# Kernel tuning notes

Measured on AMD Instinct MI355X. Metric: run time of the kernel, lower is better.

## Reference

```python
import jax, jax.numpy as jnp
import numpy as np

D = 1024


def setup_inputs() -> dict:
    key = jax.random.key(0)
    kx, kq, kk, kv, ko = jax.random.split(key, 5)
    scale = 0.02
    x = jax.random.normal(kx, (4, 2048, D), dtype=jnp.float32)
    Wq = jax.random.normal(kq, (D, D), dtype=jnp.float32) * scale
    Wk = jax.random.normal(kk, (D, D), dtype=jnp.float32) * scale
    Wv = jax.random.normal(kv, (D, D), dtype=jnp.float32) * scale
    Wo = jax.random.normal(ko, (D, D), dtype=jnp.float32) * scale
    return {"x": x, "Wq": Wq, "Wk": Wk, "Wv": Wv, "Wo": Wo}


def reference(x, Wq, Wk, Wv, Wo):
    # Linear projections (torch Linear: y = x @ W.T, no bias)
    q = jnp.einsum('bsd,ed->bse', x, Wq)
    k = jnp.einsum('bsd,ed->bse', x, Wk)
    v = jnp.einsum('bsd,ed->bse', x, Wv)
    d = x.shape[-1]
    # HRR binding: circular convolution of k and v along feature dim (rfft domain)
    Fk = jnp.fft.rfft(k, axis=-1)
    Fv = jnp.fft.rfft(v, axis=-1)
    Fq = jnp.fft.rfft(q, axis=-1)
    Fkv = Fk * Fv                      # bound key-value pairs, Fourier domain
    # causal cumulative memory over sequence; FFT is linear so cumsum commutes
    Fmem = jnp.cumsum(Fkv, axis=-2)    # [b, s, d//2+1] complex
    # unbind with query: circular correlation = multiply by conj(rfft(q))
    values_hat = jnp.fft.irfft(Fmem * jnp.conj(Fq), n=d, axis=-1)
    return jnp.einsum('bsd,ed->bse', values_hat, Wo)
```

## Files before the change

kernel.cpp:

```cpp
#include <hip/hip_runtime.h>

#define D_DIM 1024
#define NF 513
#define NB 4
#define NS 2048
#define NTOK (NB * NS)
#define NCH 32
#define CHS (NS / NCH)

typedef __attribute__((ext_vector_type(8))) short short8_t;
typedef __attribute__((ext_vector_type(4))) float f32x4;

__device__ inline unsigned short f2bf(float f) {
    unsigned u = __builtin_bit_cast(unsigned, f);
    u += 0x7FFFu + ((u >> 16) & 1u);
    return (unsigned short)(u >> 16);
}
__device__ inline float bf2f(unsigned short h) {
    unsigned u = ((unsigned)h) << 16;
    return __builtin_bit_cast(float, u);
}
__device__ inline unsigned pkc(float re, float im) {
    return (unsigned)f2bf(re) | ((unsigned)f2bf(im) << 16);
}
__device__ inline float2 upc(unsigned u) {
    return make_float2(bf2f((unsigned short)(u & 0xFFFFu)), bf2f((unsigned short)(u >> 16)));
}

__global__ __launch_bounds__(256) void convert_x(const float* __restrict__ src,
                                                 unsigned short* __restrict__ dst,
                                                 int n4) {
    int i = blockIdx.x * 256 + threadIdx.x;
    int stride = gridDim.x * 256;
    for (; i < n4; i += stride) {
        float4 v = reinterpret_cast<const float4*>(src)[i];
        ushort4 o;
        o.x = f2bf(v.x); o.y = f2bf(v.y); o.z = f2bf(v.z); o.w = f2bf(v.w);
        reinterpret_cast<ushort4*>(dst)[i] = o;
    }
}

__global__ __launch_bounds__(256) void convert_w(const float* __restrict__ Wq,
                                                 const float* __restrict__ Wk,
                                                 const float* __restrict__ Wv,
                                                 const float* __restrict__ Wo,
                                                 unsigned short* __restrict__ Wqkv,
                                                 unsigned short* __restrict__ Wob) {
    int y = blockIdx.y;
    const float* src = (y == 0) ? Wq : (y == 1) ? Wk : (y == 2) ? Wv : Wo;
    unsigned short* dst = (y < 3) ? (Wqkv + (size_t)y * 1048576) : Wob;
    int i = blockIdx.x * 256 + threadIdx.x;
    float4 v = reinterpret_cast<const float4*>(src)[i];
    ushort4 o;
    o.x = f2bf(v.x); o.y = f2bf(v.y); o.z = f2bf(v.z); o.w = f2bf(v.w);
    reinterpret_cast<ushort4*>(dst)[i] = o;
}

#define BM 128
#define BN 128
#define BK 32

__device__ inline void gload_lds16(const void* g, void* l) {
    __builtin_amdgcn_global_load_lds(
        (const __attribute__((address_space(1))) void*)g,
        (__attribute__((address_space(3))) void*)l,
        16, 0, 0);
}

template <typename OutT>
__global__ __launch_bounds__(256) void gemm_bf16_nt(const unsigned short* __restrict__ A,
                                                    const unsigned short* __restrict__ B,
                                                    OutT* __restrict__ C,
                                                    int M, int N, int K) {
    __shared__ __attribute__((aligned(16))) unsigned short ldsA[3 * BM * BK];
    __shared__ __attribute__((aligned(16))) unsigned short ldsB[3 * BM * BK];
    const int tid  = threadIdx.x;
    const int wave = tid >> 6;
    const int lane = tid & 63;
    const int l15  = lane & 15;
    const int k8   = (((lane >> 4) ^ ((l15 >> 1) & 3)) << 3);
    const int wm   = (wave >> 1) * 64;
    const int wn   = (wave & 1) * 64;
    const int bm   = blockIdx.x * BM;
    const int bn   = blockIdx.y * BN;
    const int crow = tid >> 2;
    const int ccol = (((tid & 3) ^ ((tid >> 3) & 3)) << 3);
    const int NT   = K / BK;

    const unsigned short* Arow = A + (size_t)(bm + crow) * K + ccol;
    const unsigned short* Brow = B + (size_t)(bn + crow) * K + ccol;
    const size_t rstep = (size_t)64 * K;

    f32x4 acc[4][4];
#pragma unroll
    for (int i = 0; i < 4; ++i)
#pragma unroll
        for (int j = 0; j < 4; ++j)
            acc[i][j] = (f32x4){0.f, 0.f, 0.f, 0.f};

    auto STAGE = [&](int t, int b) {
        const int k0 = t * BK;
        unsigned short* la = &ldsA[b * (BM * BK) + (tid >> 2) * BK + ((tid & 3) << 3)];
        unsigned short* lb = &ldsB[b * (BM * BK) + (tid >> 2) * BK + ((tid & 3) << 3)];
        gload_lds16(Arow + k0, la);
        gload_lds16(Brow + k0, lb);
        gload_lds16(Arow + rstep + k0, la + 64 * BK);
        gload_lds16(Brow + rstep + k0, lb + 64 * BK);
    };

    STAGE(0, 0);
    STAGE(1, 1);

    for (int j = 0; j < NT; ++j) {
        const int buf = j % 3;
        if (j + 2 < NT) STAGE(j + 2, (j + 2) % 3);

        if (j + 2 < NT)      asm volatile("s_waitcnt vmcnt(8)" ::: "memory");
        else if (j + 1 < NT) asm volatile("s_waitcnt vmcnt(4)" ::: "memory");
        else                 asm volatile("s_waitcnt vmcnt(0)" ::: "memory");
        __builtin_amdgcn_s_barrier();
        asm volatile("" ::: "memory");

        const unsigned short* la = &ldsA[buf * (BM * BK)];
        const unsigned short* lb = &ldsB[buf * (BM * BK)];
        short8_t af[4], bfv[4];
#pragma unroll
        for (int mi = 0; mi < 4; ++mi)
            af[mi] = *reinterpret_cast<const short8_t*>(&la[(wm + mi * 16 + l15) * BK + k8]);
#pragma unroll
        for (int ni = 0; ni < 4; ++ni)
            bfv[ni] = *reinterpret_cast<const short8_t*>(&lb[(wn + ni * 16 + l15) * BK + k8]);

        __builtin_amdgcn_s_setprio(1);
#pragma unroll
        for (int mi = 0; mi < 4; ++mi)
#pragma unroll
            for (int ni = 0; ni < 4; ++ni)
                acc[mi][ni] = __builtin_amdgcn_mfma_f32_16x16x32_bf16(af[mi], bfv[ni], acc[mi][ni], 0, 0, 0);
        __builtin_amdgcn_s_setprio(0);

        __builtin_amdgcn_s_barrier();
        asm volatile("" ::: "memory");
    }

#pragma unroll
    for (int mi = 0; mi < 4; ++mi) {
        int rbase = bm + wm + mi * 16 + (lane >> 4) * 4;
#pragma unroll
        for (int ni = 0; ni < 4; ++ni) {
            int col = bn + wn + ni * 16 + l15;
#pragma unroll
            for (int j = 0; j < 4; ++j) {
                float v = acc[mi][ni][j];
                if constexpr (sizeof(OutT) == 4)
                    C[(size_t)(rbase + j) * N + col] = v;
                else
                    C[(size_t)(rbase + j) * N + col] = f2bf(v);
            }
        }
    }
}

__device__ inline int sw(int i) { return i ^ ((i >> 4) & 15); }

__device__ inline int dr4(int n) {
    return ((n & 3) << 8) | (((n >> 2) & 3) << 6) | (((n >> 4) & 3) << 4) |
           (((n >> 6) & 3) << 2) | ((n >> 8) & 3);
}

__device__ inline float2 cmul(float2 a, float2 b) {
    return make_float2(a.x * b.x - a.y * b.y, a.x * b.y + a.y * b.x);
}

__device__ inline void fft1024_r4(float2* X, const float2* tw, int t) {
#pragma unroll
    for (int s = 0; s < 5; ++s) {
        const int L = 1 << (2 * s);
        const int r = t & (L - 1);
        const int base = ((t >> (2 * s)) << (2 * s + 2)) + r;
        float2 A  = X[sw(base)];
        float2 Bv = X[sw(base + L)];
        float2 Cv = X[sw(base + 2 * L)];
        float2 Dv = X[sw(base + 3 * L)];
        if (s != 0) {
            const int step = 1024 >> (2 * s + 2);
            Bv = cmul(Bv, tw[sw(r * step)]);
            Cv = cmul(Cv, tw[sw(2 * r * step)]);
            Dv = cmul(Dv, tw[sw(3 * r * step)]);
        }
        float2 e0 = make_float2(A.x + Cv.x, A.y + Cv.y);
        float2 e1 = make_float2(A.x - Cv.x, A.y - Cv.y);
        float2 o0 = make_float2(Bv.x + Dv.x, Bv.y + Dv.y);
        float2 o1 = make_float2(Bv.x - Dv.x, Bv.y - Dv.y);
        X[sw(base)]         = make_float2(e0.x + o0.x, e0.y + o0.y);
        X[sw(base + L)]     = make_float2(e1.x + o1.y, e1.y - o1.x);
        X[sw(base + 2 * L)] = make_float2(e0.x - o0.x, e0.y - o0.y);
        X[sw(base + 3 * L)] = make_float2(e1.x - o1.y, e1.y + o1.x);
        __syncthreads();
    }
}

__global__ __launch_bounds__(256) void twiddle_init(float2* __restrict__ twg) {
    int k = blockIdx.x * 256 + threadIdx.x;
    if (k < 768) {
        float ang = -6.283185307179586f * (float)k / 1024.0f;
        float s, c;
        sincosf(ang, &s, &c);
        twg[sw(k)] = make_float2(c, s);
    }
}

__global__ __launch_bounds__(256) void hrr_fft_fwd(const unsigned short* __restrict__ QKV,
                                                   const float2* __restrict__ twg,
                                                   unsigned* __restrict__ Fkv,
                                                   unsigned* __restrict__ Fq) {
    __shared__ __attribute__((aligned(16))) float2 X[1024];
    __shared__ __attribute__((aligned(16))) float2 twL[768];
    const int tid = threadIdx.x;
    const int t0 = blockIdx.x * 2, t1 = t0 + 1;
    for (int i = tid; i < 384; i += 256)
        reinterpret_cast<float4*>(twL)[i] = reinterpret_cast<const float4*>(twg)[i];

#pragma unroll
    for (int which = 0; which < 2; ++which) {
        const int tok = which ? t1 : t0;
        const ushort4* Kr = (const ushort4*)(QKV + (size_t)tok * 3072 + 1024);
        const ushort4* Vr = (const ushort4*)(QKV + (size_t)tok * 3072 + 2048);
        ushort4 k4 = Kr[tid], v4 = Vr[tid];
        X[sw(dr4(4 * tid + 0))] = make_float2(bf2f(k4.x), bf2f(v4.x));
        X[sw(dr4(4 * tid + 1))] = make_float2(bf2f(k4.y), bf2f(v4.y));
        X[sw(dr4(4 * tid + 2))] = make_float2(bf2f(k4.z), bf2f(v4.z));
        X[sw(dr4(4 * tid + 3))] = make_float2(bf2f(k4.w), bf2f(v4.w));
        __syncthreads();
        fft1024_r4(X, twL, tid);
        for (int j = tid; j < NF; j += 256) {
            float2 Zj = X[sw(j)];
            float2 Zm = X[sw((1024 - j) & 1023)];
            float2 Fk = make_float2(0.5f * (Zj.x + Zm.x), 0.5f * (Zj.y - Zm.y));
            float2 Fv = make_float2(0.5f * (Zj.y + Zm.y), 0.5f * (Zm.x - Zj.x));
            float2 p = cmul(Fk, Fv);
            Fkv[(size_t)tok * NF + j] = pkc(p.x, p.y);
        }
        __syncthreads();
    }
    {
        const ushort4* Q0 = (const ushort4*)(QKV + (size_t)t0 * 3072);
        const ushort4* Q1 = (const ushort4*)(QKV + (size_t)t1 * 3072);
        ushort4 a4 = Q0[tid], b4 = Q1[tid];
        X[sw(dr4(4 * tid + 0))] = make_float2(bf2f(a4.x), bf2f(b4.x));
        X[sw(dr4(4 * tid + 1))] = make_float2(bf2f(a4.y), bf2f(b4.y));
        X[sw(dr4(4 * tid + 2))] = make_float2(bf2f(a4.z), bf2f(b4.z));
        X[sw(dr4(4 * tid + 3))] = make_float2(bf2f(a4.w), bf2f(b4.w));
        __syncthreads();
        fft1024_r4(X, twL, tid);
        for (int j = tid; j < NF; j += 256) {
            float2 Zj = X[sw(j)];
            float2 Zm = X[sw((1024 - j) & 1023)];
            Fq[(size_t)t0 * NF + j] = pkc(0.5f * (Zj.x + Zm.x), 0.5f * (Zj.y - Zm.y));
            Fq[(size_t)t1 * NF + j] = pkc(0.5f * (Zj.y + Zm.y), 0.5f * (Zm.x - Zj.x));
        }
    }
}

__global__ __launch_bounds__(256) void hrr_chunk_sum(const unsigned* __restrict__ Fkv,
                                                     float2* __restrict__ part) {
    int f = blockIdx.x * 256 + threadIdx.x;
    if (f >= NF) return;
    int ch = blockIdx.y, b = blockIdx.z;
    float sx = 0.f, sy = 0.f;
    size_t base = ((size_t)b * NS + (size_t)ch * CHS) * NF + f;
    for (int i = 0; i < CHS; ++i) {
        float2 t = upc(Fkv[base + (size_t)i * NF]);
        sx += t.x; sy += t.y;
    }
    part[(size_t)(b * NCH + ch) * NF + f] = make_float2(sx, sy);
}

__global__ __launch_bounds__(256) void hrr_scan_apply(unsigned* __restrict__ Fkv,
                                                      const unsigned* __restrict__ Fq,
                                                      const float2* __restrict__ part) {
    int f = blockIdx.x * 256 + threadIdx.x;
    if (f >= NF) return;
    int ch = blockIdx.y, b = blockIdx.z;
    float rx = 0.f, ry = 0.f;
    for (int c2 = 0; c2 < ch; ++c2) {
        float2 p = part[(size_t)(b * NCH + c2) * NF + f];
        rx += p.x; ry += p.y;
    }
    size_t base = ((size_t)b * NS + (size_t)ch * CHS) * NF + f;
    for (int i = 0; i < CHS; ++i) {
        size_t idx = base + (size_t)i * NF;
        float2 kv = upc(Fkv[idx]);
        rx += kv.x; ry += kv.y;
        float2 q = upc(Fq[idx]);
        Fkv[idx] = pkc(rx * q.x + ry * q.y, ry * q.x - rx * q.y);
    }
}

__global__ __launch_bounds__(256) void hrr_ifft(const unsigned* __restrict__ U,
                                                const float2* __restrict__ twg,
                                                unsigned short* __restrict__ vhat) {
    __shared__ __attribute__((aligned(16))) float2 X[1024];
    __shared__ __attribute__((aligned(16))) float2 twL[768];
    const int tid = threadIdx.x;
    const int t0 = blockIdx.x * 2, t1 = t0 + 1;
    for (int i = tid; i < 384; i += 256)
        reinterpret_cast<float4*>(twL)[i] = reinterpret_cast<const float4*>(twg)[i];
    const unsigned* U1 = U + (size_t)t0 * NF;
    const unsigned* U2 = U + (size_t)t1 * NF;
#pragma unroll
    for (int c = 0; c < 4; ++c) {
        int j = tid + (c << 8);
        float2 Cv;
        if (j <= 512) {
            float2 u1 = upc(U1[j]), u2 = upc(U2[j]);
            Cv = make_float2(u1.x - u2.y, -u1.y - u2.x);
        } else {
            int m = 1024 - j;
            float2 u1 = upc(U1[m]), u2 = upc(U2[m]);
            Cv = make_float2(u1.x + u2.y, u1.y - u2.x);
        }
        X[sw(dr4(j))] = Cv;
    }
    __syncthreads();
    fft1024_r4(X, twL, tid);
    const float invN = 1.0f / 1024.0f;
#pragma unroll
    for (int c = 0; c < 4; ++c) {
        int n = tid + (c << 8);
        float2 w = X[sw(n)];
        vhat[(size_t)t0 * D_DIM + n] = f2bf(w.x * invN);
        vhat[(size_t)t1 * D_DIM + n] = f2bf(-w.y * invN);
    }
}

extern "C" void kernel_launch(void* const* d_in, const int* in_sizes, int n_in,
                              void* d_out, int out_size, void* d_ws, size_t ws_size,
                              hipStream_t stream) {
    const float* x  = (const float*)d_in[0];
    const float* Wq = (const float*)d_in[1];
    const float* Wk = (const float*)d_in[2];
    const float* Wv = (const float*)d_in[3];
    const float* Wo = (const float*)d_in[4];
    float* out = (float*)d_out;

    char* ws = (char*)d_ws;
    unsigned short* QKVb = (unsigned short*)(ws + 0);
    unsigned*       Fkv  = (unsigned*)      (ws + 50331648);
    unsigned*       Fq   = (unsigned*)      (ws + 67141632);
    float2*         part = (float2*)        (ws + 83951616);
    float2*         twg  = (float2*)        (ws + 84476928);
    unsigned short* Wob  = (unsigned short*)(ws + 84483072);
    unsigned short* Wqkv = (unsigned short*)(ws + 86580224);
    unsigned short* xb   = (unsigned short*)(ws + 92871680);
    unsigned short* vhat = (unsigned short*)(ws + 109648896);

    convert_x<<<2048, 256, 0, stream>>>(x, xb, NTOK * D_DIM / 4);
    convert_w<<<dim3(1024, 4), 256, 0, stream>>>(Wq, Wk, Wv, Wo, Wqkv, Wob);
    twiddle_init<<<3, 256, 0, stream>>>(twg);

    dim3 gq(NTOK / BM, 3072 / BN);
    gemm_bf16_nt<unsigned short><<<gq, 256, 0, stream>>>(xb, Wqkv, QKVb, NTOK, 3072, D_DIM);

    hrr_fft_fwd<<<NTOK / 2, 256, 0, stream>>>(QKVb, twg, Fkv, Fq);

    dim3 gs((NF + 255) / 256, NCH, NB);
    hrr_chunk_sum<<<gs, 256, 0, stream>>>(Fkv, part);
    hrr_scan_apply<<<gs, 256, 0, stream>>>(Fkv, Fq, part);

    hrr_ifft<<<NTOK / 2, 256, 0, stream>>>(Fkv, twg, vhat);

    dim3 go(NTOK / BM, D_DIM / BN);
    gemm_bf16_nt<float><<<go, 256, 0, stream>>>(vhat, Wob, out, NTOK, D_DIM, D_DIM);
}
```

Before: 174.1 us.

## Use 256x128 tile GEMM kernel for QKV projection

Adds a dedicated bf16 GEMM kernel with 256x128 block tiles, so each wave computes a 128x64 sub-tile, and uses it for the fused QKV projection. The larger tile raises arithmetic intensity and cuts global and LDS traffic per MFMA. It also drops from triple to double buffering. In exchange, register pressure rises (128 accumulator floats per lane), occupancy falls, and the grid becomes 32x24 = 768 blocks, which may fill the CUs less evenly.

```diff
diff --git a/kernel.cpp b/kernel.cpp
--- a/kernel.cpp
+++ b/kernel.cpp
@@ -56,8 +56,6 @@
     reinterpret_cast<ushort4*>(dst)[i] = o;
 }
 
-#define BM 128
-#define BN 128
 #define BK 32
 
 __device__ inline void gload_lds16(const void* g, void* l) {
@@ -66,6 +64,99 @@
         (__attribute__((address_space(3))) void*)l,
         16, 0, 0);
 }
+
+__global__ __launch_bounds__(256) void gemm_bf16_nt_big(const unsigned short* __restrict__ A,
+                                                        const unsigned short* __restrict__ B,
+                                                        unsigned short* __restrict__ C,
+                                                        int M, int N, int K) {
+    __shared__ __attribute__((aligned(16))) unsigned short ldsA[2 * 256 * BK];
+    __shared__ __attribute__((aligned(16))) unsigned short ldsB[2 * 128 * BK];
+    const int tid  = threadIdx.x;
+    const int wave = tid >> 6;
+    const int lane = tid & 63;
+    const int l15  = lane & 15;
+    const int k8   = (((lane >> 4) ^ ((l15 >> 1) & 3)) << 3);
+    const int wm   = (wave >> 1) * 128;
+    const int wn   = (wave & 1) * 64;
+    const int bm   = blockIdx.x * 256;
+    const int bn   = blockIdx.y * 128;
+    const int crow = tid >> 2;
+    const int ccol = (((tid & 3) ^ ((tid >> 3) & 3)) << 3);
+    const int NT   = K / BK;
+
+    const unsigned short* Arow = A + (size_t)(bm + crow) * K + ccol;
+    const unsigned short* Brow = B + (size_t)(bn + crow) * K + ccol;
+    const size_t rstep = (size_t)64 * K;
+
+    f32x4 acc[8][4];
+#pragma unroll
+    for (int i = 0; i < 8; ++i)
+#pragma unroll
+        for (int j = 0; j < 4; ++j)
+            acc[i][j] = (f32x4){0.f, 0.f, 0.f, 0.f};
+
+    auto STAGE = [&](int t, int b) {
+        const int k0 = t * BK;
+        unsigned short* la = &ldsA[b * (256 * BK) + (tid >> 2) * BK + ((tid & 3) << 3)];
+        unsigned short* lb = &ldsB[b * (128 * BK) + (tid >> 2) * BK + ((tid & 3) << 3)];
+        gload_lds16(Arow + k0,             la);
+        gload_lds16(Arow + rstep + k0,     la + 64 * BK);
+        gload_lds16(Arow + 2 * rstep + k0, la + 128 * BK);
+        gload_lds16(Arow + 3 * rstep + k0, la + 192 * BK);
+        gload_lds16(Brow + k0,             lb);
+        gload_lds16(Brow + rstep + k0,     lb + 64 * BK);
+    };
+
+    STAGE(0, 0);
+
+    for (int j = 0; j < NT; ++j) {
+        const int buf = j & 1;
+        if (j + 1 < NT) {
+            STAGE(j + 1, buf ^ 1);
+            asm volatile("s_waitcnt vmcnt(6)" ::: "memory");
+        } else {
+            asm volatile("s_waitcnt vmcnt(0)" ::: "memory");
+        }
+        __builtin_amdgcn_s_barrier();
+        asm volatile("" ::: "memory");
+
+        const unsigned short* la = &ldsA[buf * (256 * BK)];
+        const unsigned short* lb = &ldsB[buf * (128 * BK)];
+        short8_t af[8], bfv[4];
+#pragma unroll
+        for (int mi = 0; mi < 8; ++mi)
+            af[mi] = *reinterpret_cast<const short8_t*>(&la[(wm + mi * 16 + l15) * BK + k8]);
+#pragma unroll
+        for (int ni = 0; ni < 4; ++ni)
+            bfv[ni] = *reinterpret_cast<const short8_t*>(&lb[(wn + ni * 16 + l15) * BK + k8]);
+
+        __builtin_amdgcn_s_setprio(1);
+#pragma unroll
+        for (int mi = 0; mi < 8; ++mi)
+#pragma unroll
+            for (int ni = 0; ni < 4; ++ni)
+                acc[mi][ni] = __builtin_amdgcn_mfma_f32_16x16x32_bf16(af[mi], bfv[ni], acc[mi][ni], 0, 0, 0);
+        __builtin_amdgcn_s_setprio(0);
+
+        __builtin_amdgcn_s_barrier();
+        asm volatile("" ::: "memory");
+    }
+
+#pragma unroll
+    for (int mi = 0; mi < 8; ++mi) {
+        int rbase = bm + wm + mi * 16 + (lane >> 4) * 4;
+#pragma unroll
+        for (int ni = 0; ni < 4; ++ni) {
+            int col = bn + wn + ni * 16 + l15;
+#pragma unroll
+            for (int j = 0; j < 4; ++j)
+                C[(size_t)(rbase + j) * N + col] = f2bf(acc[mi][ni][j]);
+        }
+    }
+}
+
+#define BM 128
+#define BN 128
 
 template <typename OutT>
 __global__ __launch_bounds__(256) void gemm_bf16_nt(const unsigned short* __restrict__ A,
@@ -359,8 +450,8 @@
     convert_w<<<dim3(1024, 4), 256, 0, stream>>>(Wq, Wk, Wv, Wo, Wqkv, Wob);
     twiddle_init<<<3, 256, 0, stream>>>(twg);
 
-    dim3 gq(NTOK / BM, 3072 / BN);
-    gemm_bf16_nt<unsigned short><<<gq, 256, 0, stream>>>(xb, Wqkv, QKVb, NTOK, 3072, D_DIM);
+    dim3 gq(NTOK / 256, 3072 / 128);
+    gemm_bf16_nt_big<<<gq, 256, 0, stream>>>(xb, Wqkv, QKVb, NTOK, 3072, D_DIM);
 
     hrr_fft_fwd<<<NTOK / 2, 256, 0, stream>>>(QKVb, twg, Fkv, Fq);
 
```

Result: slower. 214.1 us (+23.0%).
